# Performance work log

Hardware: AMD Instinct MI355X
Metric: run time of the kernel (lower is better)

## Reference

```python
import jax, jax.numpy as jnp
import numpy as np

N_NODES = 100000


def _sage_conv(x, src, dst, w_self, w_neigh, b):
    # DGL SAGEConv('mean'): fc_self(x) + fc_neigh(mean of in-neighbor feats) + bias
    msgs = x[src]                                        # [E, d] gather
    agg = jax.ops.segment_sum(msgs, dst, num_segments=N_NODES)   # [N, d]
    deg = jax.ops.segment_sum(jnp.ones_like(dst, dtype=x.dtype), dst,
                              num_segments=N_NODES)      # [N]
    mean = agg / jnp.maximum(deg, 1.0)[:, None]          # zero-degree -> 0
    return x @ w_self + mean @ w_neigh + b


def setup_inputs() -> dict:
    key = jax.random.key(0)
    ks = jax.random.split(key, 8)
    E, D_IN, D_HID, D_OUT = 1000000, 64, 64, 32
    features = jax.random.normal(ks[0], (N_NODES, D_IN), dtype=jnp.float32)
    src = jax.random.randint(ks[1], (E,), 0, N_NODES, dtype=jnp.int32)
    dst = jax.random.randint(ks[2], (E,), 0, N_NODES, dtype=jnp.int32)
    s = lambda k, i, o: jax.random.normal(k, (i, o), dtype=jnp.float32) / np.sqrt(i)
    return {
        "features": features, "src": src, "dst": dst,
        "w_self1": s(ks[3], D_IN, D_HID), "w_neigh1": s(ks[4], D_IN, D_HID),
        "b1": jnp.zeros((D_HID,), jnp.float32),
        "w_self2": s(ks[5], D_HID, D_OUT), "w_neigh2": s(ks[6], D_HID, D_OUT),
        "b2": jnp.zeros((D_OUT,), jnp.float32),
    }


def reference(features, src, dst, w_self1, w_neigh1, b1, w_self2, w_neigh2, b2):
    h = _sage_conv(features, src, dst, w_self1, w_neigh1, b1)
    h = jax.nn.relu(h)
    # dropout: identity (inference mode)
    h = _sage_conv(h, src, dst, w_self2, w_neigh2, b2)
    return h
```

## Files before the change

kernel.cpp:

```cpp
#include <hip/hip_runtime.h>


#define SPAN        128
#define SPAN_SHIFT  7
#define PART_BLOCK  1024
#define PART_EPT    4
#define NBMAX       1024
#define LDS_S       72

typedef __attribute__((ext_vector_type(8))) short bf16x8;
typedef __attribute__((ext_vector_type(4))) float f32x4;

__device__ __forceinline__ unsigned bf16_rne(float f) {
    unsigned u = __float_as_uint(f);
    return (u + 0x7FFFu + ((u >> 16) & 1u)) >> 16;
}
__device__ __forceinline__ float bf_lo(unsigned u) { return __uint_as_float(u << 16); }
__device__ __forceinline__ float bf_hi(unsigned u) { return __uint_as_float(u & 0xFFFF0000u); }

__global__ __launch_bounds__(PART_BLOCK) void k_partition(
    const int* __restrict__ src, const int* __restrict__ dst,
    int* __restrict__ cursor, unsigned int* __restrict__ pairs,
    int E, int cap,
    const float* __restrict__ feat, unsigned short* __restrict__ xh, long total8,
    const float* __restrict__ ws1, const float* __restrict__ wn1,
    const float* __restrict__ ws2, const float* __restrict__ wn2,
    unsigned short* __restrict__ wt)
{
    const int tid = threadIdx.x;
    for (long i = (long)blockIdx.x * PART_BLOCK + tid; i < total8;
         i += (long)gridDim.x * PART_BLOCK) {
        const float4 a = ((const float4*)feat)[i * 2];
        const float4 b = ((const float4*)feat)[i * 2 + 1];
        uint4 o;
        o.x = bf16_rne(a.x) | (bf16_rne(a.y) << 16);
        o.y = bf16_rne(a.z) | (bf16_rne(a.w) << 16);
        o.z = bf16_rne(b.x) | (bf16_rne(b.y) << 16);
        o.w = bf16_rne(b.z) | (bf16_rne(b.w) << 16);
        ((uint4*)xh)[i] = o;
    }
    if (blockIdx.x < 12) {
        int j = blockIdx.x * PART_BLOCK + tid;
        int mat = j >> 12, rem = j & 4095;
        int c = rem >> 6, k = rem & 63;
        float v;
        if (mat == 0)      v = ws1[k * 64 + c];
        else if (mat == 1) v = wn1[k * 64 + c];
        else               v = (c < 32) ? wn2[k * 32 + c] : ws2[k * 32 + (c - 32)];
        wt[(mat << 12) + (c << 6) + k] = (unsigned short)bf16_rne(v);
    }

    __shared__ int cnt[NBMAX];
    __shared__ int gbase[NBMAX];
    __shared__ int lcur[NBMAX];
    cnt[tid] = 0; lcur[tid] = 0;
    __syncthreads();

    int sv[PART_EPT], bv[PART_EPT];
    const int e0 = blockIdx.x * (PART_BLOCK * PART_EPT) + tid;
    #pragma unroll
    for (int j = 0; j < PART_EPT; ++j) {
        int e = e0 + j * PART_BLOCK;
        bv[j] = -1;
        if (e < E) {
            int s = src[e], d = dst[e];
            bv[j] = d >> SPAN_SHIFT;
            sv[j] = s | ((d & (SPAN - 1)) << 24);
            atomicAdd(&cnt[bv[j]], 1);
        }
    }
    __syncthreads();
    if (cnt[tid] > 0) gbase[tid] = atomicAdd(&cursor[tid], cnt[tid]);
    __syncthreads();
    #pragma unroll
    for (int j = 0; j < PART_EPT; ++j) {
        if (bv[j] >= 0) {
            int r = gbase[bv[j]] + atomicAdd(&lcur[bv[j]], 1);
            if (r < cap) pairs[(size_t)bv[j] * cap + r] = (unsigned int)sv[j];
        }
    }
}

__global__ __launch_bounds__(256) void k_bucket_csr(
    unsigned int* __restrict__ pairs,
    const int* __restrict__ cursor,
    int* __restrict__ starts, int* __restrict__ degs,
    int N, int cap)
{
    __shared__ int cnt[SPAN];
    __shared__ int pref[SPAN];
    __shared__ int lcur[SPAN];
    extern __shared__ unsigned int sorted[];
    const int tid = threadIdx.x;
    const int b = blockIdx.x;
    if (tid < SPAN) { cnt[tid] = 0; lcur[tid] = 0; }
    __syncthreads();

    int m = cursor[b]; if (m > cap) m = cap;
    const size_t pb = (size_t)b * cap;

    for (int i = tid; i < m; i += 256)
        atomicAdd(&cnt[pairs[pb + i] >> 24], 1);
    __syncthreads();

    if (tid < SPAN) pref[tid] = cnt[tid];
    __syncthreads();
    for (int off = 1; off < SPAN; off <<= 1) {
        int v = 0;
        if (tid < SPAN && tid >= off) v = pref[tid - off];
        __syncthreads();
        if (tid < SPAN) pref[tid] += v;
        __syncthreads();
    }

    for (int i = tid; i < m; i += 256) {
        unsigned int p = pairs[pb + i];
        int r = p >> 24;
        int base = (r == 0) ? 0 : pref[r - 1];
        int pos = base + atomicAdd(&lcur[r], 1);
        sorted[pos] = p & 0xFFFFFFu;
    }
    __syncthreads();
    for (int i = tid; i < m; i += 256) pairs[pb + i] = sorted[i];
    if (tid < SPAN) {
        int node = (b << SPAN_SHIFT) + tid;
        if (node < N) {
            int base = (tid == 0) ? 0 : pref[tid - 1];
            starts[node] = (int)pb + base;
            degs[node]   = cnt[tid];
        }
    }
}

__global__ __launch_bounds__(512, 6) void k_fused(
    const unsigned short* __restrict__ xh,
    const unsigned int* __restrict__ esrc,
    const int* __restrict__ starts, const int* __restrict__ degs,
    const unsigned short* __restrict__ wt,
    const float* __restrict__ b1, const float* __restrict__ b2,
    unsigned short* __restrict__ t2,
    float* __restrict__ outp,
    int n)
{
    __shared__ __align__(16) unsigned short sM[128 * LDS_S];
    const int tid  = threadIdx.x;
    const int w    = tid >> 6, lane = tid & 63;
    const int quad = lane >> 4, lm = lane & 15;
    const int gm0  = blockIdx.x * 128;
    const int rowW = w * 16;

    for (int grp = 0; grp < 4; ++grp) {
        const int v0 = gm0 + rowW + grp * 4;
        int e[4], end[4], dg[4];
        #pragma unroll
        for (int j = 0; j < 4; ++j) {
            int v = v0 + j;
            if (v < n) { int b = starts[v]; dg[j] = degs[v]; e[j] = b + quad; end[j] = b + dg[j]; }
            else { dg[j] = 0; e[j] = 0; end[j] = 0; }
        }
        float ga[4][4];
        #pragma unroll
        for (int j = 0; j < 4; ++j)
            #pragma unroll
            for (int k = 0; k < 4; ++k) ga[j][k] = 0.f;

        while ((e[0] < end[0]) | (e[1] < end[1]) | (e[2] < end[2]) | (e[3] < end[3])) {
            uint2 u[4]; float m[4];
            #pragma unroll
            for (int j = 0; j < 4; ++j) {
                bool p = e[j] < end[j];
                m[j] = p ? 1.f : 0.f;
                int idx = p ? e[j] : 0;
                int s = (int)(esrc[idx] & 0xFFFFFFu);
                s = s < n ? s : n - 1;
                u[j] = *(const uint2*)&xh[(size_t)s * 64 + lm * 4];
            }
            #pragma unroll
            for (int j = 0; j < 4; ++j) {
                ga[j][0] = fmaf(m[j], bf_lo(u[j].x), ga[j][0]);
                ga[j][1] = fmaf(m[j], bf_hi(u[j].x), ga[j][1]);
                ga[j][2] = fmaf(m[j], bf_lo(u[j].y), ga[j][2]);
                ga[j][3] = fmaf(m[j], bf_hi(u[j].y), ga[j][3]);
                e[j] += 4;
            }
        }
        #pragma unroll
        for (int j = 0; j < 4; ++j) {
            #pragma unroll
            for (int d = 16; d <= 32; d <<= 1) {
                #pragma unroll
                for (int k = 0; k < 4; ++k) ga[j][k] += __shfl_xor(ga[j][k], d);
            }
            if (lane < 16 && v0 + j < n) {
                float f = dg[j] ? 1.f / (float)dg[j] : 0.f;
                uint2 o;
                o.x = bf16_rne(ga[j][0] * f) | (bf16_rne(ga[j][1] * f) << 16);
                o.y = bf16_rne(ga[j][2] * f) | (bf16_rne(ga[j][3] * f) << 16);
                *(uint2*)&sM[(rowW + grp * 4 + j) * LDS_S + lm * 4] = o;
            }
        }
    }

    f32x4 acc[4];
    #pragma unroll
    for (int nt = 0; nt < 4; ++nt) acc[nt] = (f32x4){0.f, 0.f, 0.f, 0.f};

    const int rowG = gm0 + rowW + lm;
    const int rA = rowG < n ? rowG : n - 1;
    #pragma unroll
    for (int kt = 0; kt < 2; ++kt) {
        bf16x8 a  = *(const bf16x8*)&xh[(size_t)rA * 64 + kt * 32 + quad * 8];
        bf16x8 am = *(const bf16x8*)&sM[(rowW + lm) * LDS_S + kt * 32 + quad * 8];
        #pragma unroll
        for (int nt = 0; nt < 4; ++nt) {
            bf16x8 bs = *(const bf16x8*)&wt[((nt * 16 + lm) << 6) + kt * 32 + quad * 8];
            bf16x8 bn = *(const bf16x8*)&wt[(1 << 12) + ((nt * 16 + lm) << 6) + kt * 32 + quad * 8];
            acc[nt] = __builtin_amdgcn_mfma_f32_16x16x32_bf16(a,  bs, acc[nt], 0, 0, 0);
            acc[nt] = __builtin_amdgcn_mfma_f32_16x16x32_bf16(am, bn, acc[nt], 0, 0, 0);
        }
    }

    #pragma unroll
    for (int nt = 0; nt < 4; ++nt) {
        float bb = b1[nt * 16 + lm];
        int rbase = rowW + quad * 4;
        #pragma unroll
        for (int r = 0; r < 4; ++r) {
            float hv = fmaxf(acc[nt][r] + bb, 0.f);
            sM[(rbase + r) * LDS_S + nt * 16 + lm] = (unsigned short)bf16_rne(hv);
        }
    }

    f32x4 acc2[4];
    #pragma unroll
    for (int nt = 0; nt < 4; ++nt) acc2[nt] = (f32x4){0.f, 0.f, 0.f, 0.f};
    #pragma unroll
    for (int kt = 0; kt < 2; ++kt) {
        bf16x8 a = *(const bf16x8*)&sM[(rowW + lm) * LDS_S + kt * 32 + quad * 8];
        #pragma unroll
        for (int nt = 0; nt < 4; ++nt) {
            bf16x8 b = *(const bf16x8*)&wt[(2 << 12) + ((nt * 16 + lm) << 6) + kt * 32 + quad * 8];
            acc2[nt] = __builtin_amdgcn_mfma_f32_16x16x32_bf16(a, b, acc2[nt], 0, 0, 0);
        }
    }

    {
        int rbase = gm0 + rowW + quad * 4;
        #pragma unroll
        for (int nt = 0; nt < 2; ++nt) {
            #pragma unroll
            for (int r = 0; r < 4; ++r) {
                int gm = rbase + r;
                if (gm < n)
                    t2[(size_t)gm * 32 + nt * 16 + lm] =
                        (unsigned short)bf16_rne(acc2[nt][r]);
            }
        }
        #pragma unroll
        for (int nt = 2; nt < 4; ++nt) {
            float bb = b2[(nt - 2) * 16 + lm];
            #pragma unroll
            for (int r = 0; r < 4; ++r) {
                int gm = rbase + r;
                if (gm < n)
                    outp[(size_t)gm * 32 + (nt - 2) * 16 + lm] = acc2[nt][r] + bb;
            }
        }
    }
}

__global__ __launch_bounds__(256) void k_gather_b32add(
    const unsigned short* __restrict__ t2,
    const unsigned int* __restrict__ esrc,
    const int* __restrict__ starts, const int* __restrict__ degs,
    float* __restrict__ outp, int n)
{
    const int w = threadIdx.x >> 6, lane = threadIdx.x & 63;
    const int g = lane >> 3, c = lane & 7;
    const int v0 = (blockIdx.x * 4 + w) * 4;
    if (v0 >= n) return;

    int e[4], end[4], deg[4];
    #pragma unroll
    for (int j = 0; j < 4; ++j) {
        int v = v0 + j;
        if (v < n) { int b = starts[v]; deg[j] = degs[v]; e[j] = b + g; end[j] = b + deg[j]; }
        else { deg[j] = 0; e[j] = 0; end[j] = 0; }
    }
    float acc[4][4];
    #pragma unroll
    for (int j = 0; j < 4; ++j)
        #pragma unroll
        for (int k = 0; k < 4; ++k) acc[j][k] = 0.f;

    while ((e[0] < end[0]) | (e[1] < end[1]) | (e[2] < end[2]) | (e[3] < end[3])) {
        uint2 u[4]; float m[4];
        #pragma unroll
        for (int j = 0; j < 4; ++j) {
            bool p = e[j] < end[j];
            m[j] = p ? 1.f : 0.f;
            int idx = p ? e[j] : 0;
            int s = (int)(esrc[idx] & 0xFFFFFFu);
            s = s < n ? s : n - 1;
            u[j] = *(const uint2*)&t2[(size_t)s * 32 + c * 4];
        }
        #pragma unroll
        for (int j = 0; j < 4; ++j) {
            acc[j][0] = fmaf(m[j], bf_lo(u[j].x), acc[j][0]);
            acc[j][1] = fmaf(m[j], bf_hi(u[j].x), acc[j][1]);
            acc[j][2] = fmaf(m[j], bf_lo(u[j].y), acc[j][2]);
            acc[j][3] = fmaf(m[j], bf_hi(u[j].y), acc[j][3]);
            e[j] += 8;
        }
    }
    #pragma unroll
    for (int j = 0; j < 4; ++j) {
        #pragma unroll
        for (int d = 8; d <= 32; d <<= 1) {
            #pragma unroll
            for (int k = 0; k < 4; ++k) acc[j][k] += __shfl_xor(acc[j][k], d);
        }
        if (lane < 8 && v0 + j < n && deg[j] > 0) {
            float f = 1.f / (float)deg[j];
            float4 o = *(const float4*)&outp[(size_t)(v0 + j) * 32 + c * 4];
            o.x += acc[j][0] * f; o.y += acc[j][1] * f;
            o.z += acc[j][2] * f; o.w += acc[j][3] * f;
            *(float4*)&outp[(size_t)(v0 + j) * 32 + c * 4] = o;
        }
    }
}

extern "C" void kernel_launch(void* const* d_in, const int* in_sizes, int n_in,
                              void* d_out, int out_size, void* d_ws, size_t ws_size,
                              hipStream_t stream) {
    const float* feat = (const float*)d_in[0];
    const int*   src  = (const int*)d_in[1];
    const int*   dst  = (const int*)d_in[2];
    const float* ws1  = (const float*)d_in[3];
    const float* wn1  = (const float*)d_in[4];
    const float* b1   = (const float*)d_in[5];
    const float* ws2  = (const float*)d_in[6];
    const float* wn2  = (const float*)d_in[7];
    const float* b2   = (const float*)d_in[8];
    float* out = (float*)d_out;

    const int N = in_sizes[0] / 64;
    const int E = in_sizes[1];
    const int nB = (N + SPAN - 1) >> SPAN_SHIFT;

    int cap = ((E + nB - 1) / nB);
    cap = ((cap + cap / 4) + 63) & ~63;
    {
        size_t fixedBytes = NBMAX * 4 + 3 * 4096 * 2 + (size_t)N * 8
                          + (size_t)N * 64 * 2
                          + (size_t)N * 32 * 2
                          + 16384;
        size_t remain = (ws_size > fixedBytes) ? (ws_size - fixedBytes) : 0;
        size_t capMax = remain / ((size_t)nB * 4);
        if ((size_t)cap > capMax) cap = (int)(capMax & ~(size_t)3);
    }

    char* base = (char*)d_ws;
    int* cursor = (int*)base;
    unsigned short* wt = (unsigned short*)(base + NBMAX * 4);
    unsigned int* pairs = (unsigned int*)(base + NBMAX * 4 + 24576);
    size_t sOff = ((size_t)NBMAX * 4 + 24576 + (size_t)nB * cap * 4 + 4096 + 255) & ~(size_t)255;
    int* starts = (int*)(base + sOff);
    int* degs   = starts + N;
    size_t mOff = (sOff + (size_t)N * 8 + 255) & ~(size_t)255;
    unsigned short* xh = (unsigned short*)(base + mOff);
    unsigned short* t2 = xh + (size_t)N * 64;

    hipMemsetAsync(cursor, 0, NBMAX * 4, stream);

    const long total8 = (long)N * 64 / 8;
    const int pblocks = (E + PART_BLOCK * PART_EPT - 1) / (PART_BLOCK * PART_EPT);
    k_partition<<<pblocks, PART_BLOCK, 0, stream>>>(
        src, dst, cursor, pairs, E, cap,
        feat, xh, total8, ws1, wn1, ws2, wn2, wt);
    k_bucket_csr<<<nB, 256, (size_t)cap * 4, stream>>>(pairs, cursor, starts, degs, N, cap);

    const int gblocks = (N + 15) / 16;
    const int tblocks = (N + 127) / 128;

    k_fused<<<tblocks, 512, 0, stream>>>(xh, pairs, starts, degs, wt, b1, b2, t2, out, N);
    k_gather_b32add<<<gblocks, 256, 0, stream>>>(t2, pairs, starts, degs, out, N);
}
```

Baseline: 199.0 us.

## Shrink fused gather+MLP kernel to 16-node blocks with per-wave output tiles

The fused layer-1 kernel previously used 512-thread blocks covering 128 nodes, with each wave gathering four groups of four nodes serially and then computing all four output column tiles itself. It now uses 256-thread blocks covering 16 nodes: each wave gathers four nodes once, then after a block barrier each wave computes one 16-column MFMA tile for both layers. This shortens per-wave serial gather chains and increases block count and occupancy, which should hide irregular gather latency better. The cost is extra __syncthreads, more redundant weight loads per node, and smaller blocks.

```diff
diff --git a/kernel.cpp b/kernel.cpp
--- a/kernel.cpp
+++ b/kernel.cpp
@@ -132,7 +132,7 @@
     }
 }
 
-__global__ __launch_bounds__(512, 6) void k_fused(
+__global__ __launch_bounds__(256) void k_gather_fused(
     const unsigned short* __restrict__ xh,
     const unsigned int* __restrict__ esrc,
     const int* __restrict__ starts, const int* __restrict__ degs,
@@ -142,129 +142,106 @@
     float* __restrict__ outp,
     int n)
 {
-    __shared__ __align__(16) unsigned short sM[128 * LDS_S];
-    const int tid  = threadIdx.x;
-    const int w    = tid >> 6, lane = tid & 63;
+    __shared__ __align__(16) unsigned short sM[16 * LDS_S];
+    __shared__ __align__(16) unsigned short sH[16 * LDS_S];
+    const int w = threadIdx.x >> 6, lane = threadIdx.x & 63;
     const int quad = lane >> 4, lm = lane & 15;
-    const int gm0  = blockIdx.x * 128;
-    const int rowW = w * 16;
-
-    for (int grp = 0; grp < 4; ++grp) {
-        const int v0 = gm0 + rowW + grp * 4;
-        int e[4], end[4], dg[4];
+    const int gm0  = blockIdx.x * 16;
+    const int v0   = gm0 + w * 4;
+
+    int e[4], end[4], dg[4];
+    #pragma unroll
+    for (int j = 0; j < 4; ++j) {
+        int v = v0 + j;
+        if (v < n) { int b = starts[v]; dg[j] = degs[v]; e[j] = b + quad; end[j] = b + dg[j]; }
+        else { dg[j] = 0; e[j] = 0; end[j] = 0; }
+    }
+    float ga[4][4];
+    #pragma unroll
+    for (int j = 0; j < 4; ++j)
+        #pragma unroll
+        for (int k = 0; k < 4; ++k) ga[j][k] = 0.f;
+
+    while ((e[0] < end[0]) | (e[1] < end[1]) | (e[2] < end[2]) | (e[3] < end[3])) {
+        uint2 u[4]; float m[4];
         #pragma unroll
         for (int j = 0; j < 4; ++j) {
-            int v = v0 + j;
-            if (v < n) { int b = starts[v]; dg[j] = degs[v]; e[j] = b + quad; end[j] = b + dg[j]; }
-            else { dg[j] = 0; e[j] = 0; end[j] = 0; }
-        }
-        float ga[4][4];
-        #pragma unroll
-        for (int j = 0; j < 4; ++j)
+            bool p = e[j] < end[j];
+            m[j] = p ? 1.f : 0.f;
+            int idx = p ? e[j] : 0;
+            int s = (int)(esrc[idx] & 0xFFFFFFu);
+            s = s < n ? s : n - 1;
+            u[j] = *(const uint2*)&xh[(size_t)s * 64 + lm * 4];
+        }
+        #pragma unroll
+        for (int j = 0; j < 4; ++j) {
+            ga[j][0] = fmaf(m[j], bf_lo(u[j].x), ga[j][0]);
+            ga[j][1] = fmaf(m[j], bf_hi(u[j].x), ga[j][1]);
+            ga[j][2] = fmaf(m[j], bf_lo(u[j].y), ga[j][2]);
+            ga[j][3] = fmaf(m[j], bf_hi(u[j].y), ga[j][3]);
+            e[j] += 4;
+        }
+    }
+    #pragma unroll
+    for (int j = 0; j < 4; ++j) {
+        #pragma unroll
+        for (int d = 16; d <= 32; d <<= 1) {
             #pragma unroll
-            for (int k = 0; k < 4; ++k) ga[j][k] = 0.f;
-
-        while ((e[0] < end[0]) | (e[1] < end[1]) | (e[2] < end[2]) | (e[3] < end[3])) {
-            uint2 u[4]; float m[4];
-            #pragma unroll
-            for (int j = 0; j < 4; ++j) {
-                bool p = e[j] < end[j];
-                m[j] = p ? 1.f : 0.f;
-                int idx = p ? e[j] : 0;
-                int s = (int)(esrc[idx] & 0xFFFFFFu);
-                s = s < n ? s : n - 1;
-                u[j] = *(const uint2*)&xh[(size_t)s * 64 + lm * 4];
-            }
-            #pragma unroll
-            for (int j = 0; j < 4; ++j) {
-                ga[j][0] = fmaf(m[j], bf_lo(u[j].x), ga[j][0]);
-                ga[j][1] = fmaf(m[j], bf_hi(u[j].x), ga[j][1]);
-                ga[j][2] = fmaf(m[j], bf_lo(u[j].y), ga[j][2]);
-                ga[j][3] = fmaf(m[j], bf_hi(u[j].y), ga[j][3]);
-                e[j] += 4;
-            }
-        }
-        #pragma unroll
-        for (int j = 0; j < 4; ++j) {
-            #pragma unroll
-            for (int d = 16; d <= 32; d <<= 1) {
-                #pragma unroll
-                for (int k = 0; k < 4; ++k) ga[j][k] += __shfl_xor(ga[j][k], d);
-            }
-            if (lane < 16 && v0 + j < n) {
-                float f = dg[j] ? 1.f / (float)dg[j] : 0.f;
-                uint2 o;
-                o.x = bf16_rne(ga[j][0] * f) | (bf16_rne(ga[j][1] * f) << 16);
-                o.y = bf16_rne(ga[j][2] * f) | (bf16_rne(ga[j][3] * f) << 16);
-                *(uint2*)&sM[(rowW + grp * 4 + j) * LDS_S + lm * 4] = o;
-            }
-        }
-    }
-
-    f32x4 acc[4];
-    #pragma unroll
-    for (int nt = 0; nt < 4; ++nt) acc[nt] = (f32x4){0.f, 0.f, 0.f, 0.f};
-
-    const int rowG = gm0 + rowW + lm;
+            for (int k = 0; k < 4; ++k) ga[j][k] += __shfl_xor(ga[j][k], d);
+        }
+        if (lane < 16) {
+            float f = dg[j] ? 1.f / (float)dg[j] : 0.f;
+            uint2 o;
+            o.x = bf16_rne(ga[j][0] * f) | (bf16_rne(ga[j][1] * f) << 16);
+            o.y = bf16_rne(ga[j][2] * f) | (bf16_rne(ga[j][3] * f) << 16);
+            *(uint2*)&sM[(w * 4 + j) * LDS_S + lm * 4] = o;
+        }
+    }
+    __syncthreads();
+
+    f32x4 acc1 = (f32x4){0.f, 0.f, 0.f, 0.f};
+    const int rowG = gm0 + lm;
     const int rA = rowG < n ? rowG : n - 1;
     #pragma unroll
     for (int kt = 0; kt < 2; ++kt) {
         bf16x8 a  = *(const bf16x8*)&xh[(size_t)rA * 64 + kt * 32 + quad * 8];
-        bf16x8 am = *(const bf16x8*)&sM[(rowW + lm) * LDS_S + kt * 32 + quad * 8];
-        #pragma unroll
-        for (int nt = 0; nt < 4; ++nt) {
-            bf16x8 bs = *(const bf16x8*)&wt[((nt * 16 + lm) << 6) + kt * 32 + quad * 8];
-            bf16x8 bn = *(const bf16x8*)&wt[(1 << 12) + ((nt * 16 + lm) << 6) + kt * 32 + quad * 8];
-            acc[nt] = __builtin_amdgcn_mfma_f32_16x16x32_bf16(a,  bs, acc[nt], 0, 0, 0);
-            acc[nt] = __builtin_amdgcn_mfma_f32_16x16x32_bf16(am, bn, acc[nt], 0, 0, 0);
-        }
-    }
-
-    #pragma unroll
-    for (int nt = 0; nt < 4; ++nt) {
-        float bb = b1[nt * 16 + lm];
-        int rbase = rowW + quad * 4;
+        bf16x8 am = *(const bf16x8*)&sM[lm * LDS_S + kt * 32 + quad * 8];
+        bf16x8 bs = *(const bf16x8*)&wt[((w * 16 + lm) << 6) + kt * 32 + quad * 8];
+        bf16x8 bn = *(const bf16x8*)&wt[(1 << 12) + ((w * 16 + lm) << 6) + kt * 32 + quad * 8];
+        acc1 = __builtin_amdgcn_mfma_f32_16x16x32_bf16(a,  bs, acc1, 0, 0, 0);
+        acc1 = __builtin_amdgcn_mfma_f32_16x16x32_bf16(am, bn, acc1, 0, 0, 0);
+    }
+    {
+        float bb = b1[w * 16 + lm];
         #pragma unroll
         for (int r = 0; r < 4; ++r) {
-            float hv = fmaxf(acc[nt][r] + bb, 0.f);
-            sM[(rbase + r) * LDS_S + nt * 16 + lm] = (unsigned short)bf16_rne(hv);
-        }
-    }
-
-    f32x4 acc2[4];
-    #pragma unroll
-    for (int nt = 0; nt < 4; ++nt) acc2[nt] = (f32x4){0.f, 0.f, 0.f, 0.f};
+            float hv = fmaxf(acc1[r] + bb, 0.f);
+            sH[(quad * 4 + r) * LDS_S + w * 16 + lm] = (unsigned short)bf16_rne(hv);
+        }
+    }
+    __syncthreads();
+
+    f32x4 acc2 = (f32x4){0.f, 0.f, 0.f, 0.f};
     #pragma unroll
     for (int kt = 0; kt < 2; ++kt) {
-        bf16x8 a = *(const bf16x8*)&sM[(rowW + lm) * LDS_S + kt * 32 + quad * 8];
-        #pragma unroll
-        for (int nt = 0; nt < 4; ++nt) {
-            bf16x8 b = *(const bf16x8*)&wt[(2 << 12) + ((nt * 16 + lm) << 6) + kt * 32 + quad * 8];
-            acc2[nt] = __builtin_amdgcn_mfma_f32_16x16x32_bf16(a, b, acc2[nt], 0, 0, 0);
-        }
-    }
-
-    {
-        int rbase = gm0 + rowW + quad * 4;
-        #pragma unroll
-        for (int nt = 0; nt < 2; ++nt) {
-            #pragma unroll
-            for (int r = 0; r < 4; ++r) {
-                int gm = rbase + r;
-                if (gm < n)
-                    t2[(size_t)gm * 32 + nt * 16 + lm] =
-                        (unsigned short)bf16_rne(acc2[nt][r]);
-            }
-        }
-        #pragma unroll
-        for (int nt = 2; nt < 4; ++nt) {
-            float bb = b2[(nt - 2) * 16 + lm];
-            #pragma unroll
-            for (int r = 0; r < 4; ++r) {
-                int gm = rbase + r;
-                if (gm < n)
-                    outp[(size_t)gm * 32 + (nt - 2) * 16 + lm] = acc2[nt][r] + bb;
-            }
+        bf16x8 a = *(const bf16x8*)&sH[lm * LDS_S + kt * 32 + quad * 8];
+        bf16x8 b = *(const bf16x8*)&wt[(2 << 12) + ((w * 16 + lm) << 6) + kt * 32 + quad * 8];
+        acc2 = __builtin_amdgcn_mfma_f32_16x16x32_bf16(a, b, acc2, 0, 0, 0);
+    }
+    if (w < 2) {
+        #pragma unroll
+        for (int r = 0; r < 4; ++r) {
+            int gm = gm0 + quad * 4 + r;
+            if (gm < n)
+                t2[(size_t)gm * 32 + w * 16 + lm] = (unsigned short)bf16_rne(acc2[r]);
+        }
+    } else {
+        float bb = b2[(w - 2) * 16 + lm];
+        #pragma unroll
+        for (int r = 0; r < 4; ++r) {
+            int gm = gm0 + quad * 4 + r;
+            if (gm < n)
+                outp[(size_t)gm * 32 + (w - 2) * 16 + lm] = acc2[r] + bb;
         }
     }
 }
@@ -381,8 +358,8 @@
     k_bucket_csr<<<nB, 256, (size_t)cap * 4, stream>>>(pairs, cursor, starts, degs, N, cap);
 
     const int gblocks = (N + 15) / 16;
-    const int tblocks = (N + 127) / 128;
-
-    k_fused<<<tblocks, 512, 0, stream>>>(xh, pairs, starts, degs, wt, b1, b2, t2, out, N);
+
+    k_gather_fused<<<gblocks, 256, 0, stream>>>(
+        xh, pairs, starts, degs, wt, b1, b2, t2, out, N);
     k_gather_b32add<<<gblocks, 256, 0, stream>>>(t2, pairs, starts, degs, out, N);
 }
```

Result: faster. 184.0 us (-7.5%).
